# Kernel optimization log

Hardware: AMD Instinct MI355X
Metric: run time of the kernel (lower is better)

The kernel has to match this reference:

```python
import jax, jax.numpy as jnp
import numpy as np

B, S, D, H = 2, 2048, 1024, 16
HD = D // H  # head dim = 64


def setup_inputs() -> dict:
    key = jax.random.key(0)
    ks = jax.random.split(key, 9)
    s_in = 1.0 / np.sqrt(D)
    s_out = 1.0 / np.sqrt(HD)
    return {
        "x": jax.random.normal(ks[0], (B, S, D), jnp.float32),
        "Wq": jax.random.normal(ks[1], (D, H, HD), jnp.float32) * s_in,
        "bq": jnp.zeros((H, HD), jnp.float32),
        "Wk": jax.random.normal(ks[2], (D, H, HD), jnp.float32) * s_in,
        "bk": jnp.zeros((H, HD), jnp.float32),
        "Wv": jax.random.normal(ks[3], (D, H, HD), jnp.float32) * s_in,
        "bv": jnp.zeros((H, HD), jnp.float32),
        "Wo": jax.random.normal(ks[4], (H, HD, D), jnp.float32) * s_out,
        "bo": jnp.zeros((D,), jnp.float32),
    }


def reference(x, Wq, bq, Wk, bk, Wv, bv, Wo, bo):
    # QKV projections: [B,S,D] -> [B,S,H,HD]
    q = jnp.einsum("bsd,dhk->bshk", x, Wq) + bq
    k = jnp.einsum("bsd,dhk->bshk", x, Wk) + bk
    v = jnp.einsum("bsd,dhk->bshk", x, Wv) + bv

    # scaled dot-product attention (matches nnx.dot_product_attention)
    scale = jnp.asarray(1.0 / np.sqrt(HD), q.dtype)
    scores = jnp.einsum("bqhk,bshk->bhqs", q * scale, k)  # [B,H,S,S]
    attn = jax.nn.softmax(scores, axis=-1)
    y = jnp.einsum("bhqs,bshk->bqhk", attn, v)  # [B,S,H,HD]

    # exclusive post-processing: subtract projection onto L2-normalized v
    eps = jnp.asarray(1e-12, v.dtype)
    v_norm = v * jax.lax.rsqrt(jnp.sum(jnp.square(v), axis=-1, keepdims=True) + eps)
    y = y - jnp.sum(y * v_norm, axis=-1, keepdims=True) * v_norm

    # output projection: [B,S,H,HD] -> [B,S,D]
    out = jnp.einsum("bshk,hkd->bsd", y, Wo) + bo
    return out  # dropout is identity (deterministic=True)
```

## Files before the change

### kernel.cpp

```cpp
#include <hip/hip_runtime.h>

#define BB 2
#define SS 2048
#define DD 1024
#define HH 16
#define HDD 64

typedef __attribute__((ext_vector_type(4))) float f32x4;
typedef __attribute__((ext_vector_type(8))) short short8;
typedef __attribute__((ext_vector_type(4))) short short4v;

__device__ __forceinline__ short f2bf(float f) {
    union { float f; unsigned u; } a; a.f = f;
    unsigned r = a.u + 0x7fffu + ((a.u >> 16) & 1u);
    return (short)(r >> 16);
}
__device__ __forceinline__ float bf2f(short s) {
    union { unsigned u; float f; } a; a.u = ((unsigned)(unsigned short)s) << 16;
    return a.f;
}
__device__ __forceinline__ float fast_exp2(float x) {
    float r;
    asm("v_exp_f32 %0, %1\n\ts_nop 0" : "=v"(r) : "v"(x));
    return r;
}
__device__ __forceinline__ unsigned cvt_pk_bf16(float lo, float hi) {
    unsigned r;
    asm("v_cvt_pk_bf16_f32 %0, %1, %2" : "=v"(r) : "v"(lo), "v"(hi));
    return r;
}

#define GLD16(gp, lp) __builtin_amdgcn_global_load_lds( \
    (const __attribute__((address_space(1))) void*)(gp), \
    (__attribute__((address_space(3))) void*)(lp), 16, 0, 0)

__global__ __launch_bounds__(256) void conv_all(
    const float* __restrict__ x,
    const float* __restrict__ Wq, const float* __restrict__ Wk,
    const float* __restrict__ Wv, const float* __restrict__ Wo,
    short* __restrict__ xb, short* __restrict__ Wt, short* __restrict__ Wot,
    float qscale)
{
    const int z = blockIdx.z;
    if (z == 4) {
        const int id = blockIdx.x * 16 + blockIdx.y;
        const size_t base = (size_t)id * 16384 + threadIdx.x * 8;
        #pragma unroll
        for (int it = 0; it < 8; ++it) {
            const size_t i = base + (size_t)it * 2048;
            f32x4 a = *(const f32x4*)(x + i);
            f32x4 b = *(const f32x4*)(x + i + 4);
            short8 o;
            #pragma unroll
            for (int j = 0; j < 4; j++) { o[j] = f2bf(a[j]); o[j + 4] = f2bf(b[j]); }
            *(short8*)(xb + i) = o;
        }
        return;
    }
    __shared__ float t[64][65];
    const float* src = (z == 0) ? Wq : (z == 1) ? Wk : (z == 2) ? Wv : Wo;
    short* dst = (z < 3) ? (Wt + (size_t)z * 1048576) : Wot;
    const float scale = (z == 0) ? qscale : 1.f;

    const int tid = threadIdx.x;
    const int c = tid & 63, rg = tid >> 6;
    const int bi = blockIdx.x * 64, bj = blockIdx.y * 64;
    #pragma unroll
    for (int i = 0; i < 16; i++)
        t[rg * 16 + i][c] = src[(size_t)(bi + rg * 16 + i) * 1024 + bj + c];
    __syncthreads();
    #pragma unroll
    for (int i = 0; i < 16; i++)
        dst[(size_t)(bj + rg * 16 + i) * 1024 + bi + c] = f2bf(scale * t[c][rg * 16 + i]);
}

template<int KIND>
__global__ __launch_bounds__(256, 2) void gemm_mfma(
    const short* __restrict__ A, const short* __restrict__ Bt,
    const float* __restrict__ b0, const float* __restrict__ b1,
    const float* __restrict__ b2, float qscale,
    short* __restrict__ oQ, short* __restrict__ oK, short* __restrict__ oV,
    float* __restrict__ oF)
{
    constexpr int BM = (KIND == 0) ? 128 : 64;
    constexpr int FM = BM / 32;
    constexpr int ASH = BM * 64;
    constexpr int BUFSTR = ASH + 8192;

    __shared__ short lds[2 * BUFSTR];
    const int tid = threadIdx.x;
    const int lane = tid & 63;
    const int ln15 = lane & 15, g = lane >> 4;
    const int swl = ln15 & 7;
    const int wid = tid >> 6;
    const int wm = wid >> 1, wn = wid & 1;
    const int bm = blockIdx.x * BM;
    const int bn = blockIdx.y * 128;
    const bool vpath = (KIND == 0) && (blockIdx.y >= 16);

    f32x4 acc[FM][4];
    #pragma unroll
    for (int i = 0; i < FM; i++)
        #pragma unroll
        for (int j = 0; j < 4; j++) acc[i][j] = (f32x4){0.f, 0.f, 0.f, 0.f};

    const int sr = lane >> 3, cs = lane & 7;
    const int sc8 = (cs ^ sr) << 3;
    const short* Ak = A;
    const short* Bk = Bt;
    int aoff[FM], adst[FM], boff[4], bdst[4];
    #pragma unroll
    for (int j = 0; j < FM; j++) {
        aoff[j] = (bm + wid * (BM / 4) + j * 8 + sr) * 1024 + sc8;
        adst[j] = (wid * (BM / 4) + j * 8) * 64;
    }
    #pragma unroll
    for (int j = 0; j < 4; j++) {
        boff[j] = (bn + wid * 32 + j * 8 + sr) * 1024 + sc8;
        bdst[j] = ASH + (wid * 32 + j * 8) * 64;
    }

    auto stage = [&](int BUF) {
        #pragma unroll
        for (int j = 0; j < FM; j++)
            GLD16(Ak + aoff[j], &lds[BUF * BUFSTR + adst[j]]);
        #pragma unroll
        for (int j = 0; j < 4; j++)
            GLD16(Bk + boff[j], &lds[BUF * BUFSTR + bdst[j]]);
        Ak += 64; Bk += 64;
    };

    const char* ldsc = (const char*)lds;
    int aB[2], bB[2];
    #pragma unroll
    for (int kk = 0; kk < 2; kk++) {
        aB[kk] = (wm * (BM / 2) + ln15) * 128 + ((((kk << 2) | g) ^ swl) << 4);
        bB[kk] = ASH * 2 + (wn * 64 + ln15) * 128 + ((((kk << 2) | g) ^ swl) << 4);
    }

    auto tilec = [&](int BUF) {
        #pragma unroll
        for (int kk = 0; kk < 2; kk++) {
            short8 af[FM], bf[4];
            #pragma unroll
            for (int f = 0; f < FM; f++)
                af[f] = *(const short8*)(ldsc + BUF * (BUFSTR * 2) + aB[kk] + f * 2048);
            #pragma unroll
            for (int f = 0; f < 4; f++)
                bf[f] = *(const short8*)(ldsc + BUF * (BUFSTR * 2) + bB[kk] + f * 2048);
            if (!vpath) {
                #pragma unroll
                for (int fm = 0; fm < FM; fm++)
                    #pragma unroll
                    for (int fn = 0; fn < 4; fn++)
                        acc[fm][fn] = __builtin_amdgcn_mfma_f32_16x16x32_bf16(
                            bf[fn], af[fm], acc[fm][fn], 0, 0, 0);
            } else {
                #pragma unroll
                for (int fm = 0; fm < FM; fm++)
                    #pragma unroll
                    for (int fn = 0; fn < 4; fn++)
                        acc[fm][fn] = __builtin_amdgcn_mfma_f32_16x16x32_bf16(
                            af[fm], bf[fn], acc[fm][fn], 0, 0, 0);
            }
        }
    };

    stage(0);
    asm volatile("s_waitcnt vmcnt(0)" ::: "memory");
    __builtin_amdgcn_s_barrier();

    #pragma unroll 1
    for (int i = 0; i < 7; ++i) {
        stage(1);
        tilec(0);
        asm volatile("s_waitcnt vmcnt(0) lgkmcnt(0)" ::: "memory");
        __builtin_amdgcn_s_barrier();
        stage(0);
        tilec(1);
        asm volatile("s_waitcnt vmcnt(0) lgkmcnt(0)" ::: "memory");
        __builtin_amdgcn_s_barrier();
    }
    stage(1);
    tilec(0);
    asm volatile("s_waitcnt vmcnt(0) lgkmcnt(0)" ::: "memory");
    __builtin_amdgcn_s_barrier();
    tilec(1);

    const int n_base = bn + wn * 64;

    if constexpr (KIND == 1) {
        #pragma unroll
        for (int fn = 0; fn < 4; fn++) {
            const int n0 = n_base + fn * 16 + 4 * g;
            const f32x4 b4 = *(const f32x4*)(b0 + n0);
            #pragma unroll
            for (int fm = 0; fm < FM; fm++) {
                const int t = bm + wm * (BM / 2) + fm * 16 + ln15;
                f32x4 o = acc[fm][fn] + b4;
                *(f32x4*)(oF + (size_t)t * 1024 + n0) = o;
            }
        }
    } else if (!vpath) {
        const bool isq = (n_base < 1024);
        short* dst = isq ? oQ : oK;
        const float* bp = isq ? b0 : b1;
        const float scl = isq ? qscale : 1.f;
        #pragma unroll
        for (int fn = 0; fn < 4; fn++) {
            const int n0 = n_base + fn * 16 + 4 * g;
            const int nl = n0 & 1023;
            f32x4 b4 = *(const f32x4*)(bp + nl);
            b4 *= scl;
            const int h = nl >> 6, d = nl & 63;
            #pragma unroll
            for (int fm = 0; fm < FM; fm++) {
                const int t = bm + wm * (BM / 2) + fm * 16 + ln15;
                const int b = t >> 11, s = t & 2047;
                short4v pk = { f2bf(acc[fm][fn][0] + b4[0]), f2bf(acc[fm][fn][1] + b4[1]),
                               f2bf(acc[fm][fn][2] + b4[2]), f2bf(acc[fm][fn][3] + b4[3]) };
                *(short4v*)(dst + ((size_t)(b * HH + h) * SS + s) * HDD + d) = pk;
            }
        }
    } else {
        #pragma unroll
        for (int fn = 0; fn < 4; fn++) {
            const int nf = n_base + fn * 16 + ln15;
            const int nl = nf - 2048;
            const float bb = b2[nl];
            const int h = nl >> 6, d = nl & 63;
            #pragma unroll
            for (int fm = 0; fm < FM; fm++) {
                const int t0 = bm + wm * (BM / 2) + fm * 16 + 4 * g;
                const int b = t0 >> 11;
                const int sb = (t0 & 2047) & ~63;
                const int pos = g * 16 + (fm & 1) * 4 + ((fm >> 1) & 1) * 8;
                short4v pk = { f2bf(acc[fm][fn][0] + bb), f2bf(acc[fm][fn][1] + bb),
                               f2bf(acc[fm][fn][2] + bb), f2bf(acc[fm][fn][3] + bb) };
                *(short4v*)(oV + ((size_t)(b * HH + h) * HDD + d) * SS + sb + pos) = pk;
            }
        }
    }
}

__global__ __launch_bounds__(256, 2) void attn_mfma_kernel(
    const short* __restrict__ Qh, const short* __restrict__ Kh,
    const short* __restrict__ Vt, short* __restrict__ yb)
{
    __shared__ short lds[32768];

    const int lane = threadIdx.x & 63;
    const int wid  = threadIdx.x >> 6;
    const int ln15 = lane & 15;
    const int g    = lane >> 4;
    const int swl  = ln15 & 7;

    const int bid  = ((int)blockIdx.x & 7) * 64 + ((int)blockIdx.x >> 3);
    const int bh   = bid >> 4;
    const int qB   = (bid & 15) * 128;
    const int qW   = qB + wid * 32;

    const short* qbase = Qh + (size_t)bh * SS * HDD;
    const short* kbase = Kh + (size_t)bh * SS * HDD;
    const short* vtb   = Vt + (size_t)bh * HDD * SS;

    short8 qf[2][2];
    #pragma unroll
    for (int qg = 0; qg < 2; qg++)
        #pragma unroll
        for (int c = 0; c < 2; c++)
            qf[qg][c] = *(const short8*)(qbase +
                (size_t)(qW + qg * 16 + ln15) * HDD + c * 32 + g * 8);

    const short8 ones = { 0x3f80, 0x3f80, 0x3f80, 0x3f80,
                          0x3f80, 0x3f80, 0x3f80, 0x3f80 };

    const int sr = lane >> 3;
    const int cs = lane & 7;
    const int sc8 = (cs ^ sr) << 3;
    const int rvl = lane >> 4;
    const int cc = lane & 15;
    const short* Kk = kbase;
    const short* Vk = vtb;
    int koff[4], kdst[4], voff[4], vdst[4];
    #pragma unroll
    for (int j = 0; j < 4; j++) {
        koff[j] = (wid * 32 + j * 8 + sr) * 64 + sc8;
        kdst[j] = (wid * 32 + j * 8) * 64;
        const int rv = wid * 16 + j * 4 + rvl;
        voff[j] = rv * 2048 + ((cc ^ (rv & 7)) << 3);
        vdst[j] = 8192 + (wid * 16 + j * 4) * 128;
    }

    auto stage = [&](const int BUF) {
        #pragma unroll
        for (int j = 0; j < 4; j++)
            GLD16(Kk + koff[j], &lds[BUF * 16384 + kdst[j]]);
        #pragma unroll
        for (int j = 0; j < 4; j++)
            GLD16(Vk + voff[j], &lds[BUF * 16384 + vdst[j]]);
        Kk += 8192; Vk += 128;
    };

    const char* ldsc = (const char*)lds;
    const int kA0 = ln15 * 128 + ((g ^ swl) << 4);
    const int kA1 = ln15 * 128 + (((4 + g) ^ swl) << 4);
    const int vA0 = 16384 + ln15 * 256 + (((2 * g) ^ swl) << 4);
    const int vA1 = 16384 + ln15 * 256 + (((2 * g + 1) ^ swl) << 4);

    f32x4 o[2][4], ol[2];
    #pragma unroll
    for (int qg = 0; qg < 2; qg++) {
        ol[qg] = (f32x4){0.f, 0.f, 0.f, 0.f};
        #pragma unroll
        for (int c = 0; c < 4; c++) o[qg][c] = (f32x4){0.f, 0.f, 0.f, 0.f};
    }

    union Pk { unsigned u[4]; short8 v; };
    Pk PA0[2], PA1[2], PB0[2], PB1[2];

    auto qkexp = [&](const int BUF) {
        const char* base = ldsc + BUF * 32768;
        f32x4 s[8][2];
        const f32x4 z = {0.f, 0.f, 0.f, 0.f};
        __builtin_amdgcn_s_setprio(1);
        #pragma unroll
        for (int kg = 0; kg < 8; kg++) {
            const short8 k0 = *(const short8*)(base + kA0 + kg * 2048);
            const short8 k1 = *(const short8*)(base + kA1 + kg * 2048);
            #pragma unroll
            for (int qg = 0; qg < 2; qg++) {
                s[kg][qg] = __builtin_amdgcn_mfma_f32_16x16x32_bf16(
                    k0, qf[qg][0], z, 0, 0, 0);
                s[kg][qg] = __builtin_amdgcn_mfma_f32_16x16x32_bf16(
                    k1, qf[qg][1], s[kg][qg], 0, 0, 0);
            }
        }
        __builtin_amdgcn_s_setprio(0);

        #pragma unroll
        for (int qg = 0; qg < 2; qg++) {
            float p[32];
            #pragma unroll
            for (int kg = 0; kg < 8; kg++)
                #pragma unroll
                for (int r = 0; r < 4; r++)
                    p[kg * 4 + r] = fast_exp2(s[kg][qg][r]);
            PA0[qg].u[0] = cvt_pk_bf16(p[0], p[1]);
            PA0[qg].u[1] = cvt_pk_bf16(p[2], p[3]);
            PA0[qg].u[2] = cvt_pk_bf16(p[4], p[5]);
            PA0[qg].u[3] = cvt_pk_bf16(p[6], p[7]);
            PA1[qg].u[0] = cvt_pk_bf16(p[8], p[9]);
            PA1[qg].u[1] = cvt_pk_bf16(p[10], p[11]);
            PA1[qg].u[2] = cvt_pk_bf16(p[12], p[13]);
            PA1[qg].u[3] = cvt_pk_bf16(p[14], p[15]);
            PB0[qg].u[0] = cvt_pk_bf16(p[16], p[17]);
            PB0[qg].u[1] = cvt_pk_bf16(p[18], p[19]);
            PB0[qg].u[2] = cvt_pk_bf16(p[20], p[21]);
            PB0[qg].u[3] = cvt_pk_bf16(p[22], p[23]);
            PB1[qg].u[0] = cvt_pk_bf16(p[24], p[25]);
            PB1[qg].u[1] = cvt_pk_bf16(p[26], p[27]);
            PB1[qg].u[2] = cvt_pk_bf16(p[28], p[29]);
            PB1[qg].u[3] = cvt_pk_bf16(p[30], p[31]);
        }
    };

    auto pv = [&](const int BUF) {
        const char* base = ldsc + BUF * 32768;
        __builtin_amdgcn_s_setprio(1);
        #pragma unroll
        for (int c = 0; c < 4; c++) {
            const short8 vfA0 = *(const short8*)(base + vA0 + c * 4096);
            const short8 vfA1 = *(const short8*)(base + vA1 + c * 4096);
            const short8 vfB0 = *(const short8*)(base + vA0 + c * 4096 + 128);
            const short8 vfB1 = *(const short8*)(base + vA1 + c * 4096 + 128);
            #pragma unroll
            for (int qg = 0; qg < 2; qg++) {
                o[qg][c] = __builtin_amdgcn_mfma_f32_16x16x32_bf16(
                    vfA0, PA0[qg].v, o[qg][c], 0, 0, 0);
                o[qg][c] = __builtin_amdgcn_mfma_f32_16x16x32_bf16(
                    vfA1, PA1[qg].v, o[qg][c], 0, 0, 0);
                o[qg][c] = __builtin_amdgcn_mfma_f32_16x16x32_bf16(
                    vfB0, PB0[qg].v, o[qg][c], 0, 0, 0);
                o[qg][c] = __builtin_amdgcn_mfma_f32_16x16x32_bf16(
                    vfB1, PB1[qg].v, o[qg][c], 0, 0, 0);
            }
        }
        #pragma unroll
        for (int qg = 0; qg < 2; qg++) {
            ol[qg] = __builtin_amdgcn_mfma_f32_16x16x32_bf16(ones, PA0[qg].v, ol[qg], 0, 0, 0);
            ol[qg] = __builtin_amdgcn_mfma_f32_16x16x32_bf16(ones, PA1[qg].v, ol[qg], 0, 0, 0);
            ol[qg] = __builtin_amdgcn_mfma_f32_16x16x32_bf16(ones, PB0[qg].v, ol[qg], 0, 0, 0);
            ol[qg] = __builtin_amdgcn_mfma_f32_16x16x32_bf16(ones, PB1[qg].v, ol[qg], 0, 0, 0);
        }
        __builtin_amdgcn_s_setprio(0);
    };

#define LGKM0 asm volatile("s_waitcnt lgkmcnt(0)" ::: "memory")
#define WAITV0 asm volatile("s_waitcnt vmcnt(0) lgkmcnt(0)" ::: "memory")
#define BARR __builtin_amdgcn_s_barrier()

    stage(0);
    WAITV0; BARR;
    stage(1); qkexp(0); WAITV0; BARR;

    #pragma unroll 1
    for (int i = 0; i < 7; ++i) {
        pv(0); LGKM0; BARR; stage(0); qkexp(1); WAITV0; BARR;
        pv(1); LGKM0; BARR; stage(1); qkexp(0); WAITV0; BARR;
    }
    pv(0);
    qkexp(1);
    pv(1);

#undef LGKM0
#undef WAITV0
#undef BARR

    const int b = bh >> 4, h = bh & 15;
    #pragma unroll
    for (int qg = 0; qg < 2; qg++) {
        const float inv = 1.f / ol[qg][0];
        #pragma unroll
        for (int c = 0; c < 4; c++) o[qg][c] *= inv;

        const int spos = qB + (wid >> 1) * 64 + (ln15 >> 2) * 16 + qg * 4 +
                         (wid & 1) * 8 + (ln15 & 3);
        float v4[4][4];
        float nv = 0.f, dv = 0.f;
        #pragma unroll
        for (int c = 0; c < 4; c++)
            #pragma unroll
            for (int r = 0; r < 4; r++) {
                const float vd = bf2f(vtb[(size_t)(c * 16 + 4 * g + r) * SS + spos]);
                v4[c][r] = vd;
                nv += vd * vd;
                dv += o[qg][c][r] * vd;
            }
        nv += __shfl_xor(nv, 16); nv += __shfl_xor(nv, 32);
        dv += __shfl_xor(dv, 16); dv += __shfl_xor(dv, 32);
        const float tpp = dv / (nv + 1e-12f);

        const int tok = b * SS + qW + qg * 16 + ln15;
        #pragma unroll
        for (int c = 0; c < 4; c++) {
            short4v pk = { f2bf(o[qg][c][0] - v4[c][0] * tpp),
                           f2bf(o[qg][c][1] - v4[c][1] * tpp),
                           f2bf(o[qg][c][2] - v4[c][2] * tpp),
                           f2bf(o[qg][c][3] - v4[c][3] * tpp) };
            *(short4v*)(yb + (size_t)tok * 1024 + h * 64 + c * 16 + 4 * g) = pk;
        }
    }
}

extern "C" void kernel_launch(void* const* d_in, const int* in_sizes, int n_in,
                              void* d_out, int out_size, void* d_ws, size_t ws_size,
                              hipStream_t stream)
{
    const float* x  = (const float*)d_in[0];
    const float* Wq = (const float*)d_in[1];
    const float* bq = (const float*)d_in[2];
    const float* Wk = (const float*)d_in[3];
    const float* bk = (const float*)d_in[4];
    const float* Wv = (const float*)d_in[5];
    const float* bv = (const float*)d_in[6];
    const float* Wo = (const float*)d_in[7];
    const float* bo = (const float*)d_in[8];
    float* out = (float*)d_out;

    char* w = (char*)d_ws;
    short* xb   = (short*)(w);
    short* Wt   = (short*)(w + (8ull << 20));
    short* Wot  = (short*)(w + (14ull << 20));
    short* Qh   = (short*)(w + (16ull << 20));
    short* Kh   = (short*)(w + (24ull << 20));
    short* Vt   = (short*)(w + (32ull << 20));
    short* yb   = (short*)(w + (40ull << 20));

    const float qscale = 0.125f * 1.44269504f;
    dim3 blk(256);

    conv_all<<<dim3(16, 16, 5), blk, 0, stream>>>(x, Wq, Wk, Wv, Wo,
                                                  xb, Wt, Wot, qscale);

    gemm_mfma<0><<<dim3(32, 24), blk, 0, stream>>>(xb, Wt, bq, bk, bv, qscale,
                                                   Qh, Kh, Vt, nullptr);

    attn_mfma_kernel<<<dim3(512), blk, 0, stream>>>(Qh, Kh, Vt, yb);

    gemm_mfma<1><<<dim3(64, 8), blk, 0, stream>>>(yb, Wot, bo, nullptr, nullptr, 1.f,
                                                  nullptr, nullptr, nullptr, out);
}
```

Before: 100.2 us.

## Load K fragments directly into registers and halve the attention key tile

K tiles are no longer staged through LDS. Each wave now loads its K MFMA fragments straight from global memory into registers, and only V^T goes through a smaller double-buffered LDS tile of 64 keys. This drops LDS traffic and footprint (16KB instead of 64KB) and restructures the loop into 32 smaller steps, with the K load for the next step overlapped with the current PV. The trade-off is that every wave re-reads the same K block from L2/global, and there are twice as many barriers and wait points per key sweep.

```diff
diff --git a/kernel.cpp b/kernel.cpp
--- a/kernel.cpp
+++ b/kernel.cpp
@@ -247,7 +247,7 @@
     const short* __restrict__ Qh, const short* __restrict__ Kh,
     const short* __restrict__ Vt, short* __restrict__ yb)
 {
-    __shared__ short lds[32768];
+    __shared__ short lds[8192];
 
     const int lane = threadIdx.x & 63;
     const int wid  = threadIdx.x >> 6;
@@ -278,35 +278,38 @@
     const int sr = lane >> 3;
     const int cs = lane & 7;
     const int sc8 = (cs ^ sr) << 3;
-    const int rvl = lane >> 4;
-    const int cc = lane & 15;
-    const short* Kk = kbase;
+    const int r0 = wid * 16 + sr;
+    const int r1 = r0 + 8;
     const short* Vk = vtb;
-    int koff[4], kdst[4], voff[4], vdst[4];
-    #pragma unroll
-    for (int j = 0; j < 4; j++) {
-        koff[j] = (wid * 32 + j * 8 + sr) * 64 + sc8;
-        kdst[j] = (wid * 32 + j * 8) * 64;
-        const int rv = wid * 16 + j * 4 + rvl;
-        voff[j] = rv * 2048 + ((cc ^ (rv & 7)) << 3);
-        vdst[j] = 8192 + (wid * 16 + j * 4) * 128;
-    }
+    const int voff0 = r0 * 2048 + sc8, voff1 = r1 * 2048 + sc8;
+    const int d0 = wid * 1024, d1 = d0 + 512;
 
     auto stage = [&](const int BUF) {
-        #pragma unroll
-        for (int j = 0; j < 4; j++)
-            GLD16(Kk + koff[j], &lds[BUF * 16384 + kdst[j]]);
-        #pragma unroll
-        for (int j = 0; j < 4; j++)
-            GLD16(Vk + voff[j], &lds[BUF * 16384 + vdst[j]]);
-        Kk += 8192; Vk += 128;
+        GLD16(Vk + voff0, &lds[BUF * 4096 + d0]);
+        GLD16(Vk + voff1, &lds[BUF * 4096 + d1]);
+        Vk += 64;
+    };
+
+    const short* Kp = kbase;
+    int kO[4][2];
+    #pragma unroll
+    for (int kg = 0; kg < 4; kg++) {
+        kO[kg][0] = (kg * 16 + ln15) * 64 + g * 8;
+        kO[kg][1] = kO[kg][0] + 32;
+    }
+    short8 kf[4][2];
+    auto kload = [&]() {
+        #pragma unroll
+        for (int kg = 0; kg < 4; kg++) {
+            kf[kg][0] = *(const short8*)(Kp + kO[kg][0]);
+            kf[kg][1] = *(const short8*)(Kp + kO[kg][1]);
+        }
+        Kp += 4096;
     };
 
     const char* ldsc = (const char*)lds;
-    const int kA0 = ln15 * 128 + ((g ^ swl) << 4);
-    const int kA1 = ln15 * 128 + (((4 + g) ^ swl) << 4);
-    const int vA0 = 16384 + ln15 * 256 + (((2 * g) ^ swl) << 4);
-    const int vA1 = 16384 + ln15 * 256 + (((2 * g + 1) ^ swl) << 4);
+    const int vA0 = ln15 * 128 + (((2 * g) ^ swl) << 4);
+    const int vA1 = ln15 * 128 + (((2 * g + 1) ^ swl) << 4);
 
     f32x4 o[2][4], ol[2];
     #pragma unroll
@@ -317,103 +320,80 @@
     }
 
     union Pk { unsigned u[4]; short8 v; };
-    Pk PA0[2], PA1[2], PB0[2], PB1[2];
-
-    auto qkexp = [&](const int BUF) {
-        const char* base = ldsc + BUF * 32768;
-        f32x4 s[8][2];
+    Pk P0[2], P1[2];
+
+    auto qkexp = [&]() {
+        f32x4 s[4][2];
         const f32x4 z = {0.f, 0.f, 0.f, 0.f};
         __builtin_amdgcn_s_setprio(1);
         #pragma unroll
-        for (int kg = 0; kg < 8; kg++) {
-            const short8 k0 = *(const short8*)(base + kA0 + kg * 2048);
-            const short8 k1 = *(const short8*)(base + kA1 + kg * 2048);
+        for (int kg = 0; kg < 4; kg++)
             #pragma unroll
             for (int qg = 0; qg < 2; qg++) {
                 s[kg][qg] = __builtin_amdgcn_mfma_f32_16x16x32_bf16(
-                    k0, qf[qg][0], z, 0, 0, 0);
+                    kf[kg][0], qf[qg][0], z, 0, 0, 0);
                 s[kg][qg] = __builtin_amdgcn_mfma_f32_16x16x32_bf16(
-                    k1, qf[qg][1], s[kg][qg], 0, 0, 0);
-            }
-        }
+                    kf[kg][1], qf[qg][1], s[kg][qg], 0, 0, 0);
+            }
         __builtin_amdgcn_s_setprio(0);
 
         #pragma unroll
         for (int qg = 0; qg < 2; qg++) {
-            float p[32];
-            #pragma unroll
-            for (int kg = 0; kg < 8; kg++)
+            float p[16];
+            #pragma unroll
+            for (int kg = 0; kg < 4; kg++)
                 #pragma unroll
                 for (int r = 0; r < 4; r++)
                     p[kg * 4 + r] = fast_exp2(s[kg][qg][r]);
-            PA0[qg].u[0] = cvt_pk_bf16(p[0], p[1]);
-            PA0[qg].u[1] = cvt_pk_bf16(p[2], p[3]);
-            PA0[qg].u[2] = cvt_pk_bf16(p[4], p[5]);
-            PA0[qg].u[3] = cvt_pk_bf16(p[6], p[7]);
-            PA1[qg].u[0] = cvt_pk_bf16(p[8], p[9]);
-            PA1[qg].u[1] = cvt_pk_bf16(p[10], p[11]);
-            PA1[qg].u[2] = cvt_pk_bf16(p[12], p[13]);
-            PA1[qg].u[3] = cvt_pk_bf16(p[14], p[15]);
-            PB0[qg].u[0] = cvt_pk_bf16(p[16], p[17]);
-            PB0[qg].u[1] = cvt_pk_bf16(p[18], p[19]);
-            PB0[qg].u[2] = cvt_pk_bf16(p[20], p[21]);
-            PB0[qg].u[3] = cvt_pk_bf16(p[22], p[23]);
-            PB1[qg].u[0] = cvt_pk_bf16(p[24], p[25]);
-            PB1[qg].u[1] = cvt_pk_bf16(p[26], p[27]);
-            PB1[qg].u[2] = cvt_pk_bf16(p[28], p[29]);
-            PB1[qg].u[3] = cvt_pk_bf16(p[30], p[31]);
+            P0[qg].u[0] = cvt_pk_bf16(p[0], p[1]);
+            P0[qg].u[1] = cvt_pk_bf16(p[2], p[3]);
+            P0[qg].u[2] = cvt_pk_bf16(p[4], p[5]);
+            P0[qg].u[3] = cvt_pk_bf16(p[6], p[7]);
+            P1[qg].u[0] = cvt_pk_bf16(p[8], p[9]);
+            P1[qg].u[1] = cvt_pk_bf16(p[10], p[11]);
+            P1[qg].u[2] = cvt_pk_bf16(p[12], p[13]);
+            P1[qg].u[3] = cvt_pk_bf16(p[14], p[15]);
         }
     };
 
     auto pv = [&](const int BUF) {
-        const char* base = ldsc + BUF * 32768;
+        const char* base = ldsc + BUF * 8192;
         __builtin_amdgcn_s_setprio(1);
         #pragma unroll
         for (int c = 0; c < 4; c++) {
-            const short8 vfA0 = *(const short8*)(base + vA0 + c * 4096);
-            const short8 vfA1 = *(const short8*)(base + vA1 + c * 4096);
-            const short8 vfB0 = *(const short8*)(base + vA0 + c * 4096 + 128);
-            const short8 vfB1 = *(const short8*)(base + vA1 + c * 4096 + 128);
+            const short8 vf0 = *(const short8*)(base + vA0 + c * 2048);
+            const short8 vf1 = *(const short8*)(base + vA1 + c * 2048);
             #pragma unroll
             for (int qg = 0; qg < 2; qg++) {
                 o[qg][c] = __builtin_amdgcn_mfma_f32_16x16x32_bf16(
-                    vfA0, PA0[qg].v, o[qg][c], 0, 0, 0);
+                    vf0, P0[qg].v, o[qg][c], 0, 0, 0);
                 o[qg][c] = __builtin_amdgcn_mfma_f32_16x16x32_bf16(
-                    vfA1, PA1[qg].v, o[qg][c], 0, 0, 0);
-                o[qg][c] = __builtin_amdgcn_mfma_f32_16x16x32_bf16(
-                    vfB0, PB0[qg].v, o[qg][c], 0, 0, 0);
-                o[qg][c] = __builtin_amdgcn_mfma_f32_16x16x32_bf16(
-                    vfB1, PB1[qg].v, o[qg][c], 0, 0, 0);
+                    vf1, P1[qg].v, o[qg][c], 0, 0, 0);
             }
         }
         #pragma unroll
         for (int qg = 0; qg < 2; qg++) {
-            ol[qg] = __builtin_amdgcn_mfma_f32_16x16x32_bf16(ones, PA0[qg].v, ol[qg], 0, 0, 0);
-            ol[qg] = __builtin_amdgcn_mfma_f32_16x16x32_bf16(ones, PA1[qg].v, ol[qg], 0, 0, 0);
-            ol[qg] = __builtin_amdgcn_mfma_f32_16x16x32_bf16(ones, PB0[qg].v, ol[qg], 0, 0, 0);
-            ol[qg] = __builtin_amdgcn_mfma_f32_16x16x32_bf16(ones, PB1[qg].v, ol[qg], 0, 0, 0);
+            ol[qg] = __builtin_amdgcn_mfma_f32_16x16x32_bf16(ones, P0[qg].v, ol[qg], 0, 0, 0);
+            ol[qg] = __builtin_amdgcn_mfma_f32_16x16x32_bf16(ones, P1[qg].v, ol[qg], 0, 0, 0);
         }
         __builtin_amdgcn_s_setprio(0);
     };
 
-#define LGKM0 asm volatile("s_waitcnt lgkmcnt(0)" ::: "memory")
 #define WAITV0 asm volatile("s_waitcnt vmcnt(0) lgkmcnt(0)" ::: "memory")
 #define BARR __builtin_amdgcn_s_barrier()
 
     stage(0);
+    kload();
     WAITV0; BARR;
-    stage(1); qkexp(0); WAITV0; BARR;
 
     #pragma unroll 1
-    for (int i = 0; i < 7; ++i) {
-        pv(0); LGKM0; BARR; stage(0); qkexp(1); WAITV0; BARR;
-        pv(1); LGKM0; BARR; stage(1); qkexp(0); WAITV0; BARR;
-    }
-    pv(0);
-    qkexp(1);
-    pv(1);
-
-#undef LGKM0
+    for (int i = 0; i < 15; ++i) {
+        stage(1); qkexp(); kload(); pv(0); WAITV0; BARR;
+        stage(0); qkexp(); kload(); pv(1); WAITV0; BARR;
+    }
+    stage(1); qkexp(); kload(); pv(0); WAITV0; BARR;
+    qkexp(); pv(1);
+
 #undef WAITV0
 #undef BARR
 
```

Measured after the change: 135.2 us. 35.0% more time.
